# Optimization experiments

Measured on AMD Instinct MI355X. Metric: run time of the kernel, lower is better.

## Reference

```python
import jax, jax.numpy as jnp
import numpy as np

DIM = 4096
N_HEADS = 32
HEAD_DIM = 128
N_KV_HEADS = 8
REPEAT = N_HEADS // N_KV_HEADS  # 4
B = 8
# ragged per-sequence lengths, fixed so total token count is static (jit-friendly)
SEQLEN = np.array([1024, 3072, 2048, 2560, 1536, 2048, 1792, 2304], dtype=np.int64)
TOTAL = int(SEQLEN.sum())  # 16384


def setup_inputs() -> dict:
    key = jax.random.key(0)
    k1, k2, k3 = jax.random.split(key, 3)
    embedding = jax.random.normal(k1, (B, DIM), dtype=jnp.float32)
    # nn.Linear weights: stored as [out_features, in_features]
    W_up = jax.random.normal(k2, (N_KV_HEADS * HEAD_DIM, DIM), dtype=jnp.float32) * (DIM ** -0.5)
    W_down = jax.random.normal(k3, (DIM, N_HEADS * HEAD_DIM), dtype=jnp.float32) * ((N_HEADS * HEAD_DIM) ** -0.5)
    seqlen = jnp.asarray(SEQLEN)
    return {"embedding": embedding, "W_up": W_up, "W_down": W_down, "seqlen": seqlen}


def reference(embedding, W_up, W_down, seqlen):
    # up-projection: [B, dim] -> [B, n_kv_heads*head_dim]
    x = embedding @ W_up.T
    # split kv heads and repeat-interleave to n_heads: [B, n_kv, hd] -> [B, n_heads, hd]
    xv = x.reshape(B, N_KV_HEADS, HEAD_DIM)
    val = jnp.repeat(xv, REPEAT, axis=1).reshape(B, N_HEADS * HEAD_DIM)  # [B, dim]
    # ragged broadcast: row i repeated seqlen[i] times -> [TOTAL, dim]
    out = jnp.repeat(val, seqlen, axis=0, total_repeat_length=TOTAL)
    # down-projection on every token row (redundant per-sequence math, as in original)
    return out @ W_down.T  # [TOTAL, dim]
```

## Files before the change

kernel.cpp:

```cpp
#include <hip/hip_runtime.h>

#define DIM   4096
#define KVDIM 1024
#define NB    8
#define TOTAL 16384
#define BCAST_BLOCKS 8192

__global__ __launch_bounds__(256)
void k_up(const float* __restrict__ emb, const float* __restrict__ wup,
          float* __restrict__ x) {
    int wid  = blockIdx.x * 4 + (threadIdx.x >> 6);
    int lane = threadIdx.x & 63;
    int j = wid >> 3;
    int b = wid & 7;
    const float4* e = (const float4*)(emb + b * DIM);
    const float4* w = (const float4*)(wup + (long)j * DIM);
    float acc = 0.f;
    #pragma unroll
    for (int ii = 0; ii < 16; ii++) {
        int it = ii * 64 + lane;
        float4 ev = e[it], wv = w[it];
        acc += ev.x * wv.x + ev.y * wv.y + ev.z * wv.z + ev.w * wv.w;
    }
    #pragma unroll
    for (int off = 32; off; off >>= 1) acc += __shfl_down(acc, off, 64);
    if (lane == 0) x[b * KVDIM + j] = acc;
}

__global__ __launch_bounds__(256)
void k_down(const float* __restrict__ x, const float* __restrict__ wdn,
            float* __restrict__ y) {
    __shared__ float part[4][NB];
    int o    = blockIdx.x;
    int wv   = threadIdx.x >> 6;
    int lane = threadIdx.x & 63;
    const float4* w = (const float4*)(wdn + (long)o * DIM);

    float4 wr[4];
    int kvi[4];
    #pragma unroll
    for (int ii = 0; ii < 4; ii++) {
        int it = wv * 256 + ii * 64 + lane;
        wr[ii] = w[it];
        int k0 = it * 4;
        kvi[ii] = ((k0 >> 9) << 7) + (k0 & 127);
    }

    float acc[NB];
    #pragma unroll
    for (int b = 0; b < NB; b++) acc[b] = 0.f;
    #pragma unroll
    for (int ii = 0; ii < 4; ii++) {
        float4 wvv = wr[ii];
        #pragma unroll
        for (int b = 0; b < NB; b++) {
            const float4 xv = *(const float4*)(x + b * KVDIM + kvi[ii]);
            acc[b] += xv.x * wvv.x + xv.y * wvv.y + xv.z * wvv.z + xv.w * wvv.w;
        }
    }
    #pragma unroll
    for (int b = 0; b < NB; b++) {
        #pragma unroll
        for (int off = 32; off; off >>= 1) acc[b] += __shfl_down(acc[b], off, 64);
    }
    if (lane == 0) {
        #pragma unroll
        for (int b = 0; b < NB; b++) part[wv][b] = acc[b];
    }
    __syncthreads();
    if (threadIdx.x < NB) {
        int b = threadIdx.x;
        y[b * DIM + o] = part[0][b] + part[1][b] + part[2][b] + part[3][b];
    }
}

__global__ __launch_bounds__(256)
void k_bcast(const float* __restrict__ y, const int* __restrict__ seqlen,
             float4* __restrict__ out) {
    int c0 = seqlen[0];
    int c1 = c0 + seqlen[1];
    int c2 = c1 + seqlen[2];
    int c3 = c2 + seqlen[3];
    int c4 = c3 + seqlen[4];
    int c5 = c4 + seqlen[5];
    int c6 = c5 + seqlen[6];
    #pragma unroll
    for (int g = 0; g < TOTAL / BCAST_BLOCKS; g++) {
        int row = blockIdx.x + g * BCAST_BLOCKS;
        int s = (row >= c0) + (row >= c1) + (row >= c2) + (row >= c3)
              + (row >= c4) + (row >= c5) + (row >= c6);
        const float4* yr = (const float4*)(y + s * DIM);
        float4* orow = out + (long)row * (DIM / 4);
        #pragma unroll
        for (int c = threadIdx.x; c < DIM / 4; c += 256)
            orow[c] = yr[c];
    }
}

extern "C" void kernel_launch(void* const* d_in, const int* in_sizes, int n_in,
                              void* d_out, int out_size, void* d_ws, size_t ws_size,
                              hipStream_t stream) {
    const float* emb = (const float*)d_in[0];
    const float* wup = (const float*)d_in[1];
    const float* wdn = (const float*)d_in[2];
    const int* seqlen = (const int*)d_in[3];

    float* x = (float*)d_ws;
    float* y = x + NB * KVDIM;

    k_up   <<<NB * KVDIM / 4, 256, 0, stream>>>(emb, wup, x);
    k_down <<<DIM,            256, 0, stream>>>(x, wdn, y);
    k_bcast<<<BCAST_BLOCKS,   256, 0, stream>>>(y, seqlen, (float4*)d_out);
}
```

Baseline: 343.4 us.

## Stage x in LDS for down-proj and use nontemporal multi-row broadcast stores

The down-projection now stages the whole 8x1024 x matrix in shared memory, and each wave computes one full output column instead of four waves splitting one, which removes the cross-wave reduction. The broadcast kernel now has each thread write 16 consecutive rows from a cached register value with nontemporal stores, reloading y only when the sequence index changes. The aim is to cut redundant global reads and cache pollution in the store-bound 256 MB output write. The trade-off is that each block loads 32 KB of x into LDS, and k_down runs with 4x fewer blocks.

```diff
diff --git a/kernel.cpp b/kernel.cpp
--- a/kernel.cpp
+++ b/kernel.cpp
@@ -4,7 +4,8 @@
 #define KVDIM 1024
 #define NB    8
 #define TOTAL 16384
-#define BCAST_BLOCKS 8192
+
+typedef float f4 __attribute__((ext_vector_type(4)));
 
 __global__ __launch_bounds__(256)
 void k_up(const float* __restrict__ emb, const float* __restrict__ wup,
@@ -30,31 +31,32 @@
 __global__ __launch_bounds__(256)
 void k_down(const float* __restrict__ x, const float* __restrict__ wdn,
             float* __restrict__ y) {
-    __shared__ float part[4][NB];
-    int o    = blockIdx.x;
+    __shared__ float xs[NB * KVDIM];
+    const float4* xg = (const float4*)x;
+    float4* xs4 = (float4*)xs;
+    #pragma unroll
+    for (int i = 0; i < 8; i++)
+        xs4[threadIdx.x + i * 256] = xg[threadIdx.x + i * 256];
+    __syncthreads();
+
     int wv   = threadIdx.x >> 6;
     int lane = threadIdx.x & 63;
+    int o    = blockIdx.x * 4 + wv;
     const float4* w = (const float4*)(wdn + (long)o * DIM);
-
-    float4 wr[4];
-    int kvi[4];
-    #pragma unroll
-    for (int ii = 0; ii < 4; ii++) {
-        int it = wv * 256 + ii * 64 + lane;
-        wr[ii] = w[it];
-        int k0 = it * 4;
-        kvi[ii] = ((k0 >> 9) << 7) + (k0 & 127);
-    }
 
     float acc[NB];
     #pragma unroll
     for (int b = 0; b < NB; b++) acc[b] = 0.f;
+
     #pragma unroll
-    for (int ii = 0; ii < 4; ii++) {
-        float4 wvv = wr[ii];
+    for (int ii = 0; ii < 16; ii++) {
+        int it = ii * 64 + lane;
+        float4 wvv = w[it];
+        int k0  = it * 4;
+        int kvi = ((k0 >> 9) << 7) + (k0 & 127);
         #pragma unroll
         for (int b = 0; b < NB; b++) {
-            const float4 xv = *(const float4*)(x + b * KVDIM + kvi[ii]);
+            const float4 xv = *(const float4*)(xs + b * KVDIM + kvi);
             acc[b] += xv.x * wvv.x + xv.y * wvv.y + xv.z * wvv.z + xv.w * wvv.w;
         }
     }
@@ -65,18 +67,18 @@
     }
     if (lane == 0) {
         #pragma unroll
-        for (int b = 0; b < NB; b++) part[wv][b] = acc[b];
-    }
-    __syncthreads();
-    if (threadIdx.x < NB) {
-        int b = threadIdx.x;
-        y[b * DIM + o] = part[0][b] + part[1][b] + part[2][b] + part[3][b];
+        for (int b = 0; b < NB; b++) y[b * DIM + o] = acc[b];
     }
 }
 
+#define BC_ROWS 16
 __global__ __launch_bounds__(256)
 void k_bcast(const float* __restrict__ y, const int* __restrict__ seqlen,
-             float4* __restrict__ out) {
+             float* __restrict__ out) {
+    int rw  = blockIdx.x >> 2;
+    int cw  = blockIdx.x & 3;
+    int col = cw * 1024 + threadIdx.x * 4;
+
     int c0 = seqlen[0];
     int c1 = c0 + seqlen[1];
     int c2 = c1 + seqlen[2];
@@ -84,16 +86,20 @@
     int c4 = c3 + seqlen[4];
     int c5 = c4 + seqlen[5];
     int c6 = c5 + seqlen[6];
+
+    int row0 = rw * BC_ROWS;
+    int s_cur = -1;
+    f4 yv = (f4)(0.f);
     #pragma unroll
-    for (int g = 0; g < TOTAL / BCAST_BLOCKS; g++) {
-        int row = blockIdx.x + g * BCAST_BLOCKS;
+    for (int r = 0; r < BC_ROWS; r++) {
+        int row = row0 + r;
         int s = (row >= c0) + (row >= c1) + (row >= c2) + (row >= c3)
               + (row >= c4) + (row >= c5) + (row >= c6);
-        const float4* yr = (const float4*)(y + s * DIM);
-        float4* orow = out + (long)row * (DIM / 4);
-        #pragma unroll
-        for (int c = threadIdx.x; c < DIM / 4; c += 256)
-            orow[c] = yr[c];
+        if (s != s_cur) {
+            yv = *(const f4*)(y + s * DIM + col);
+            s_cur = s;
+        }
+        __builtin_nontemporal_store(yv, (f4*)(out + (long)row * DIM + col));
     }
 }
 
@@ -108,7 +114,7 @@
     float* x = (float*)d_ws;
     float* y = x + NB * KVDIM;
 
-    k_up   <<<NB * KVDIM / 4, 256, 0, stream>>>(emb, wup, x);
-    k_down <<<DIM,            256, 0, stream>>>(x, wdn, y);
-    k_bcast<<<BCAST_BLOCKS,   256, 0, stream>>>(y, seqlen, (float4*)d_out);
+    k_up   <<<NB * KVDIM / 4,            256, 0, stream>>>(emb, wup, x);
+    k_down <<<DIM / 4,                   256, 0, stream>>>(x, wdn, y);
+    k_bcast<<<(TOTAL / BC_ROWS) * 4,     256, 0, stream>>>(y, seqlen, (float*)d_out);
 }
```

Result: no change. 343.3 us (-0.0%).
